# Optimization experiments

Measured on AMD Instinct MI355X. Metric: run time of the kernel, lower is better.

The kernel has to match this reference:

```python
import jax, jax.numpy as jnp
import numpy as np

H, W = 128, 128
TANX, TANY = 0.5, 0.5
SCALE_MOD = 1.0
N = 2048
T_EPS = 1e-4          # early-termination threshold used by the CUDA kernel
ALPHA_MIN = 1.0 / 255.0


def setup_inputs() -> dict:
    key = jax.random.key(0)
    ks = jax.random.split(key, 6)
    z = jax.random.uniform(ks[0], (N,), minval=2.0, maxval=6.0)
    xy = jax.random.uniform(ks[1], (N, 2), minval=-0.8, maxval=0.8) * (z[:, None] * TANX)
    means3D = jnp.concatenate([xy, z[:, None]], axis=1).astype(jnp.float32)
    means2D = jnp.zeros((N, 3), jnp.float32)  # gradient receptacle in the original API
    opacities = (jax.random.uniform(ks[2], (N, 1)) * 0.9 + 0.05).astype(jnp.float32)
    colors_precomp = jax.random.uniform(ks[3], (N, 3)).astype(jnp.float32)
    scales = jax.random.uniform(ks[4], (N, 3), minval=0.01, maxval=0.05).astype(jnp.float32)
    q = jax.random.normal(ks[5], (N, 4))
    rotations = (q / jnp.linalg.norm(q, axis=1, keepdims=True)).astype(jnp.float32)
    bg = jnp.zeros((3,), jnp.float32)
    viewmatrix = jnp.eye(4, dtype=jnp.float32)  # camera at origin looking +z (row-vector convention)
    znear, zfar = 0.01, 100.0
    P = np.zeros((4, 4), np.float32)
    P[0, 0] = 1.0 / TANX
    P[1, 1] = 1.0 / TANY
    P[2, 2] = zfar / (zfar - znear)
    P[2, 3] = -(zfar * znear) / (zfar - znear)
    P[3, 2] = 1.0
    projmatrix = jnp.asarray(P.T)  # full view@proj, row-vector convention
    return dict(bg=bg, means3D=means3D, means2D=means2D, opacities=opacities,
                colors_precomp=colors_precomp, scales=scales, rotations=rotations,
                viewmatrix=viewmatrix, projmatrix=projmatrix)


def _quat_to_rot(q):
    r, x, y, z = q[:, 0], q[:, 1], q[:, 2], q[:, 3]
    return jnp.stack([
        jnp.stack([1 - 2 * (y * y + z * z), 2 * (x * y - r * z), 2 * (x * z + r * y)], -1),
        jnp.stack([2 * (x * y + r * z), 1 - 2 * (x * x + z * z), 2 * (y * z - r * x)], -1),
        jnp.stack([2 * (x * z - r * y), 2 * (y * z + r * x), 1 - 2 * (x * x + y * y)], -1)], -2)


def _rasterize(bg, means3D, opacities, colors, scales, rotations, viewmatrix, projmatrix):
    n = means3D.shape[0]
    mh = jnp.concatenate([means3D, jnp.ones((n, 1), means3D.dtype)], 1)
    p_view = mh @ viewmatrix                 # [N,4] camera-space position
    tz = p_view[:, 2]
    p_hom = mh @ projmatrix
    p_proj = p_hom[:, :3] / (p_hom[:, 3:4] + 1e-7)
    # 3D covariance Sigma = (R S)(R S)^T
    qn = rotations / jnp.linalg.norm(rotations, axis=1, keepdims=True)
    Rm = _quat_to_rot(qn)
    M = Rm * (scales * SCALE_MOD)[:, None, :]      # R @ diag(s)
    Sigma = jnp.einsum('nij,nkj->nik', M, M)
    # EWA projection to a 2D covariance
    fx, fy = W / (2 * TANX), H / (2 * TANY)
    tx = jnp.clip(p_view[:, 0] / tz, -1.3 * TANX, 1.3 * TANX) * tz
    ty = jnp.clip(p_view[:, 1] / tz, -1.3 * TANY, 1.3 * TANY) * tz
    zero = jnp.zeros_like(tz)
    J = jnp.stack([jnp.stack([fx / tz, zero, -fx * tx / (tz * tz)], -1),
                   jnp.stack([zero, fy / tz, -fy * ty / (tz * tz)], -1)], -2)  # [N,2,3]
    Wr = viewmatrix[:3, :3]
    cov_cam = jnp.einsum('ji,njk,kl->nil', Wr, Sigma, Wr)      # W^T Sigma W
    cov2d = jnp.einsum('nij,njk,nlk->nil', J, cov_cam, J)      # [N,2,2]
    a = cov2d[:, 0, 0] + 0.3
    c = cov2d[:, 1, 1] + 0.3
    b = cov2d[:, 0, 1]
    det = a * c - b * b
    valid = (tz > 0.2) & (det > 0.0)                            # near-plane + degenerate culling
    det_s = jnp.where(det > 0.0, det, 1.0)
    conA, conB, conC = c / det_s, -b / det_s, a / det_s         # conic (inverse 2D cov)
    mid = 0.5 * (a + c)
    lam = mid + jnp.sqrt(jnp.maximum(0.1, mid * mid - det))
    radii = jnp.where(valid, jnp.ceil(3.0 * jnp.sqrt(lam)), 0.0).astype(jnp.int32)
    # NDC -> pixel coords
    px = ((p_proj[:, 0] + 1.0) * W - 1.0) * 0.5
    py = ((p_proj[:, 1] + 1.0) * H - 1.0) * 0.5
    # global front-to-back depth sort (per-tile in the CUDA kernel)
    order = jnp.argsort(tz)
    px_s, py_s = px[order], py[order]
    cA, cB, cC = conA[order], conB[order], conC[order]
    op_s = opacities[order, 0]
    col_s = colors[order]
    tz_s = tz[order]
    val_s = valid[order]
    yy, xx = jnp.meshgrid(jnp.arange(H, dtype=means3D.dtype),
                          jnp.arange(W, dtype=means3D.dtype), indexing='ij')
    gx, gy = xx.reshape(-1, 1), yy.reshape(-1, 1)   # [P,1]
    dx = px_s[None, :] - gx                          # [P,N]
    dy = py_s[None, :] - gy
    power = -0.5 * (cA[None, :] * dx * dx + cC[None, :] * dy * dy) - cB[None, :] * dx * dy
    alpha = jnp.minimum(0.99, op_s[None, :] * jnp.exp(power))
    alpha = jnp.where((power <= 0.0) & (alpha >= ALPHA_MIN) & val_s[None, :], alpha, 0.0)
    Tinc = jnp.cumprod(1.0 - alpha, axis=1)
    T = jnp.concatenate([jnp.ones((H * W, 1), alpha.dtype), Tinc[:, :-1]], axis=1)  # exclusive transmittance
    wgt = jnp.where(T > T_EPS, alpha * T, 0.0)       # early termination
    color = wgt @ col_s + Tinc[:, -1:] * bg[None, :]  # [P,3]
    depth = wgt @ tz_s                                # [P]
    counter = jnp.sum(wgt > 0.0, axis=1).astype(jnp.int32)
    color = color.reshape(H, W, 3).transpose(2, 0, 1)
    depth = depth.reshape(1, H, W)
    counter = counter.reshape(H, W)
    return color, depth, radii, counter


def reference(bg, means3D, means2D, opacities, colors_precomp, scales, rotations, viewmatrix, projmatrix):
    # means2D is only a gradient receptacle in the original API; it does not affect the math.
    return _rasterize(bg, means3D, opacities, colors_precomp, scales, rotations, viewmatrix, projmatrix)
```

## Files before the change

kernel.cpp:

```cpp
#include <hip/hip_runtime.h>
#include <math.h>

#define N_G   2048
#define W_IMG 128
#define H_IMG 128
#define NPIX  (W_IMG * H_IMG)
#define TANX  0.5f
#define TANY  0.5f
#define ALPHA_MIN (1.0f / 255.0f)
#define T_EPS_C 1e-4f
#define NTHR  1024
#define NWAVE 16

__global__ __launch_bounds__(NTHR) void gs_fused(const float* __restrict__ means3D,
                                                 const float* __restrict__ opac,
                                                 const float* __restrict__ colors,
                                                 const float* __restrict__ scales,
                                                 const float* __restrict__ rots,
                                                 const float* __restrict__ viewm,
                                                 const float* __restrict__ projm,
                                                 const float* __restrict__ bg,
                                                 float* __restrict__ out) {
    __shared__ float4 bbx[N_G];
    __shared__ float4 pf1[N_G];
    __shared__ float4 pf2[N_G];
    __shared__ unsigned short lst[N_G];
    __shared__ unsigned short srt[N_G];
    __shared__ float4 scratch4[512];
    __shared__ float4 accv[NTHR];
    __shared__ int s_count;

    float* scr = (float*)scratch4;

    int tid = threadIdx.x;
    int bid = blockIdx.x;
    float* radii_out = out + 4 * NPIX;
    if (tid == 0) s_count = 0;

#pragma unroll
    for (int k = 0; k < N_G / NTHR; k++) {
        int i = k * NTHR + tid;

        float mx = means3D[i * 3 + 0], my = means3D[i * 3 + 1], mz = means3D[i * 3 + 2];
        float pv0 = mx * viewm[0] + my * viewm[4] + mz * viewm[8]  + viewm[12];
        float pv1 = mx * viewm[1] + my * viewm[5] + mz * viewm[9]  + viewm[13];
        float tz  = mx * viewm[2] + my * viewm[6] + mz * viewm[10] + viewm[14];

        float ph[4];
#pragma unroll
        for (int j = 0; j < 4; j++)
            ph[j] = mx * projm[0 * 4 + j] + my * projm[1 * 4 + j] + mz * projm[2 * 4 + j] + projm[3 * 4 + j];
        float inv_w = __builtin_amdgcn_rcpf(ph[3] + 1e-7f);
        float ppx = ph[0] * inv_w, ppy = ph[1] * inv_w;

        float qr = rots[i * 4 + 0], qx = rots[i * 4 + 1], qy = rots[i * 4 + 2], qz = rots[i * 4 + 3];
        float qn = __builtin_amdgcn_rsqf(qr * qr + qx * qx + qy * qy + qz * qz);
        qr *= qn; qx *= qn; qy *= qn; qz *= qn;
        float R[3][3] = {
            {1.0f - 2.0f * (qy * qy + qz * qz), 2.0f * (qx * qy - qr * qz), 2.0f * (qx * qz + qr * qy)},
            {2.0f * (qx * qy + qr * qz), 1.0f - 2.0f * (qx * qx + qz * qz), 2.0f * (qy * qz - qr * qx)},
            {2.0f * (qx * qz - qr * qy), 2.0f * (qy * qz + qr * qx), 1.0f - 2.0f * (qx * qx + qy * qy)}};

        float sc[3] = {scales[i * 3 + 0], scales[i * 3 + 1], scales[i * 3 + 2]};
        float M[3][3];
#pragma unroll
        for (int r = 0; r < 3; r++)
#pragma unroll
            for (int cx = 0; cx < 3; cx++) M[r][cx] = R[r][cx] * sc[cx];

        float Sg[3][3];
#pragma unroll
        for (int r = 0; r < 3; r++)
#pragma unroll
            for (int kk = 0; kk < 3; kk++)
                Sg[r][kk] = M[r][0] * M[kk][0] + M[r][1] * M[kk][1] + M[r][2] * M[kk][2];

        float T1[3][3];
#pragma unroll
        for (int j = 0; j < 3; j++)
#pragma unroll
            for (int l = 0; l < 3; l++)
                T1[j][l] = Sg[j][0] * viewm[0 * 4 + l] + Sg[j][1] * viewm[1 * 4 + l] + Sg[j][2] * viewm[2 * 4 + l];
        float Cc[3][3];
#pragma unroll
        for (int r = 0; r < 3; r++)
#pragma unroll
            for (int l = 0; l < 3; l++)
                Cc[r][l] = viewm[0 * 4 + r] * T1[0][l] + viewm[1 * 4 + r] * T1[1][l] + viewm[2 * 4 + r] * T1[2][l];

        const float fx = W_IMG / (2.0f * TANX), fy = H_IMG / (2.0f * TANY);
        float invtz = __builtin_amdgcn_rcpf(tz);
        float txl = fminf(fmaxf(pv0 * invtz, -1.3f * TANX), 1.3f * TANX) * tz;
        float tyl = fminf(fmaxf(pv1 * invtz, -1.3f * TANY), 1.3f * TANY) * tz;
        float a0 = fx * invtz, a2 = -fx * txl * invtz * invtz;
        float b1 = fy * invtz, b2 = -fy * tyl * invtz * invtz;

        float c00 = a0 * a0 * Cc[0][0] + 2.0f * a0 * a2 * Cc[0][2] + a2 * a2 * Cc[2][2];
        float c11 = b1 * b1 * Cc[1][1] + 2.0f * b1 * b2 * Cc[1][2] + b2 * b2 * Cc[2][2];
        float c01 = a0 * b1 * Cc[0][1] + a0 * b2 * Cc[0][2] + a2 * b1 * Cc[1][2] + a2 * b2 * Cc[2][2];

        float a = c00 + 0.3f, c = c11 + 0.3f, b = c01;
        float det = a * c - b * b;
        bool valid = (tz > 0.2f) && (det > 0.0f);
        float det_s = (det > 0.0f) ? det : 1.0f;
        float rdet = __builtin_amdgcn_rcpf(det_s);
        float conA = c * rdet, conB = -b * rdet, conC = a * rdet;
        float mid = 0.5f * (a + c);
        float lam = mid + __builtin_amdgcn_sqrtf(fmaxf(0.1f, mid * mid - det));
        float radf = valid ? ceilf(3.0f * __builtin_amdgcn_sqrtf(lam)) : 0.0f;

        float op = opac[i];
        float L = __logf(255.0f * op);
        float ex, ey;
        if (valid && L > 0.0f) {
            ex = __builtin_amdgcn_sqrtf(2.0f * L * a) + 2e-2f;
            ey = __builtin_amdgcn_sqrtf(2.0f * L * c) + 2e-2f;
        } else {
            ex = -1e9f; ey = -1e9f;
        }

        bbx[i] = make_float4(((ppx + 1.0f) * (float)W_IMG - 1.0f) * 0.5f,
                             ((ppy + 1.0f) * (float)H_IMG - 1.0f) * 0.5f, ex, ey);
        pf1[i] = make_float4(conA, conB, conC, op);
        pf2[i] = make_float4(colors[i * 3 + 0], colors[i * 3 + 1], colors[i * 3 + 2], tz);

        if (bid == 0) radii_out[i] = (float)(int)radf;
    }
    __syncthreads();

    int tilex = bid & 15, tiley = bid >> 4;
    int wave = tid >> 6, lane = tid & 63;

    {
        float tx0 = (float)(tilex << 3), ty0 = (float)(tiley << 3);
        float tx1 = tx0 + 7.0f, ty1 = ty0 + 7.0f;
#pragma unroll
        for (int cc = 0; cc < 2; cc++) {
            int gi = (wave * 2 + cc) * 64 + lane;
            float4 b = bbx[gi];
            bool pred = (b.x >= tx0 - b.z) && (b.x <= tx1 + b.z) &&
                        (b.y >= ty0 - b.w) && (b.y <= ty1 + b.w);
            unsigned long long m = __ballot(pred);
            int n = (int)__popcll(m);
            int base = 0;
            if (lane == 0 && n) base = atomicAdd(&s_count, n);
            base = __shfl(base, 0);
            if (pred)
                lst[base + (int)__popcll(m & ((1ull << lane) - 1ull))] = (unsigned short)gi;
        }
    }
    __syncthreads();
    int c = s_count;

    for (int t = tid; t < c; t += NTHR) scr[t] = pf2[lst[t]].w;
    __syncthreads();
    for (int t = tid; t < c; t += NTHR) {
        int gi = lst[t];
        float my = scr[t];
        int rank = 0;
        int j = 0;
        for (; j + 4 <= c; j += 4) {
            float4 v = scratch4[j >> 2];
            int i0 = lst[j], i1 = lst[j + 1], i2 = lst[j + 2], i3 = lst[j + 3];
            rank += (v.x < my) || (v.x == my && i0 < gi);
            rank += (v.y < my) || (v.y == my && i1 < gi);
            rank += (v.z < my) || (v.z == my && i2 < gi);
            rank += (v.w < my) || (v.w == my && i3 < gi);
        }
        for (; j < c; j++) {
            float v = scr[j];
            rank += (v < my) || (v == my && lst[j] < gi);
        }
        srt[rank] = (unsigned short)gi;
    }
    __syncthreads();

    float gx = (float)((tilex << 3) + (lane & 7));
    float gy = (float)((tiley << 3) + (lane >> 3));
    int seglen = (c + NWAVE - 1) / NWAVE;
    int s0 = wave * seglen;
    int s1 = min(c, s0 + seglen);

    float Tw = 1.0f;
    for (int t = s0; t < s1; ++t) {
        int g = srt[t];
        float4 f1 = pf1[g];
        float4 b = bbx[g];
        float dx = b.x - gx, dy = b.y - gy;
        float power = -0.5f * (f1.x * dx * dx + f1.z * dy * dy) - f1.y * dx * dy;
        if (power <= 0.0f) {
            float alpha = fminf(0.99f, f1.w * __expf(power));
            if (alpha >= ALPHA_MIN) Tw *= (1.0f - alpha);
        }
    }
    scr[wave * 64 + lane] = Tw;
    __syncthreads();

    float T0 = 1.0f;
#pragma unroll
    for (int s = 0; s < NWAVE - 1; ++s) if (s < wave) T0 *= scr[s * 64 + lane];
    float T = T0, cr = 0.0f, cg = 0.0f, cb = 0.0f, dep = 0.0f;
    int cnt = 0;
    if (!__all(T0 <= T_EPS_C)) {
        for (int t = s0; t < s1; ++t) {
            int g = srt[t];
            float4 f1 = pf1[g];
            float4 f2 = pf2[g];
            float4 b = bbx[g];
            float dx = b.x - gx, dy = b.y - gy;
            float power = -0.5f * (f1.x * dx * dx + f1.z * dy * dy) - f1.y * dx * dy;
            if (power <= 0.0f) {
                float alpha = fminf(0.99f, f1.w * __expf(power));
                if (alpha >= ALPHA_MIN) {
                    if (T > T_EPS_C) {
                        float w = alpha * T;
                        cr += w * f2.x; cg += w * f2.y; cb += w * f2.z;
                        dep += w * f2.w;
                        cnt++;
                    }
                    T *= (1.0f - alpha);
                    if (__all(T <= T_EPS_C)) break;
                }
            }
        }
    }
    accv[wave * 64 + lane] = make_float4(cr, cg, cb, dep);
    ((int*)lst)[wave * 64 + lane] = cnt;
    __syncthreads();

    if (tid < 64) {
        float crr = 0.0f, cgg = 0.0f, cbb = 0.0f, dpp = 0.0f, Tf = 1.0f;
        int cnt_t = 0;
        const int* an = (const int*)lst;
#pragma unroll
        for (int s = 0; s < NWAVE; ++s) {
            float4 a = accv[s * 64 + tid];
            crr += a.x; cgg += a.y; cbb += a.z; dpp += a.w;
            cnt_t += an[s * 64 + tid];
            Tf *= scr[s * 64 + tid];
        }
        crr += Tf * bg[0]; cgg += Tf * bg[1]; cbb += Tf * bg[2];

        int pid = ((tiley << 3) + (tid >> 3)) * W_IMG + (tilex << 3) + (tid & 7);
        out[0 * NPIX + pid] = crr;
        out[1 * NPIX + pid] = cgg;
        out[2 * NPIX + pid] = cbb;
        out[3 * NPIX + pid] = dpp;
        out[4 * NPIX + N_G + pid] = (float)cnt_t;
    }
}

extern "C" void kernel_launch(void* const* d_in, const int* in_sizes, int n_in,
                              void* d_out, int out_size, void* d_ws, size_t ws_size,
                              hipStream_t stream) {
    const float* bg      = (const float*)d_in[0];
    const float* means3D = (const float*)d_in[1];
    const float* opac    = (const float*)d_in[3];
    const float* colors  = (const float*)d_in[4];
    const float* scales  = (const float*)d_in[5];
    const float* rots    = (const float*)d_in[6];
    const float* viewm   = (const float*)d_in[7];
    const float* projm   = (const float*)d_in[8];

    gs_fused<<<256, NTHR, 0, stream>>>(means3D, opac, colors, scales, rots,
                                       viewm, projm, bg, (float*)d_out);
}
```

Baseline: 17.63 us.

## Use conservative bounding boxes and compute full covariance only for tile-culled gaussians

Each block no longer runs the full 3D-to-2D covariance chain for all 2048 gaussians. It uses a cheap conservative ellipse bound (max scale squared, view-matrix norm bound) for tile culling, then computes the full conic and colour only for gaussians that pass the cull, writing them in sorted order into compact shared arrays. Radii are split so each block computes 8 gaussians' radii. The looser bound admits more candidates into the sort and blend loops. The list is capped at 1024 entries, which could drop gaussians on dense tiles.

```diff
diff --git a/kernel.cpp b/kernel.cpp
--- a/kernel.cpp
+++ b/kernel.cpp
@@ -11,6 +11,79 @@
 #define T_EPS_C 1e-4f
 #define NTHR  1024
 #define NWAVE 16
+#define CAP   1024
+
+__device__ __forceinline__ void full_chain(int i,
+        const float* __restrict__ means3D, const float* __restrict__ opac,
+        const float* __restrict__ colors, const float* __restrict__ scales,
+        const float* __restrict__ rots, const float* __restrict__ viewm,
+        const float* __restrict__ projm,
+        float4& f1, float4& f2, float& radf) {
+    float mx = means3D[i * 3 + 0], my = means3D[i * 3 + 1], mz = means3D[i * 3 + 2];
+    float pv0 = mx * viewm[0] + my * viewm[4] + mz * viewm[8]  + viewm[12];
+    float pv1 = mx * viewm[1] + my * viewm[5] + mz * viewm[9]  + viewm[13];
+    float tz  = mx * viewm[2] + my * viewm[6] + mz * viewm[10] + viewm[14];
+
+    float qr = rots[i * 4 + 0], qx = rots[i * 4 + 1], qy = rots[i * 4 + 2], qz = rots[i * 4 + 3];
+    float qn = __builtin_amdgcn_rsqf(qr * qr + qx * qx + qy * qy + qz * qz);
+    qr *= qn; qx *= qn; qy *= qn; qz *= qn;
+    float R[3][3] = {
+        {1.0f - 2.0f * (qy * qy + qz * qz), 2.0f * (qx * qy - qr * qz), 2.0f * (qx * qz + qr * qy)},
+        {2.0f * (qx * qy + qr * qz), 1.0f - 2.0f * (qx * qx + qz * qz), 2.0f * (qy * qz - qr * qx)},
+        {2.0f * (qx * qz - qr * qy), 2.0f * (qy * qz + qr * qx), 1.0f - 2.0f * (qx * qx + qy * qy)}};
+
+    float sc[3] = {scales[i * 3 + 0], scales[i * 3 + 1], scales[i * 3 + 2]};
+    float M[3][3];
+#pragma unroll
+    for (int r = 0; r < 3; r++)
+#pragma unroll
+        for (int cx = 0; cx < 3; cx++) M[r][cx] = R[r][cx] * sc[cx];
+
+    float Sg[3][3];
+#pragma unroll
+    for (int r = 0; r < 3; r++)
+#pragma unroll
+        for (int kk = 0; kk < 3; kk++)
+            Sg[r][kk] = M[r][0] * M[kk][0] + M[r][1] * M[kk][1] + M[r][2] * M[kk][2];
+
+    float T1[3][3];
+#pragma unroll
+    for (int j = 0; j < 3; j++)
+#pragma unroll
+        for (int l = 0; l < 3; l++)
+            T1[j][l] = Sg[j][0] * viewm[0 * 4 + l] + Sg[j][1] * viewm[1 * 4 + l] + Sg[j][2] * viewm[2 * 4 + l];
+    float Cc[3][3];
+#pragma unroll
+    for (int r = 0; r < 3; r++)
+#pragma unroll
+        for (int l = 0; l < 3; l++)
+            Cc[r][l] = viewm[0 * 4 + r] * T1[0][l] + viewm[1 * 4 + r] * T1[1][l] + viewm[2 * 4 + r] * T1[2][l];
+
+    const float fx = W_IMG / (2.0f * TANX), fy = H_IMG / (2.0f * TANY);
+    float invtz = __builtin_amdgcn_rcpf(tz);
+    float txl = fminf(fmaxf(pv0 * invtz, -1.3f * TANX), 1.3f * TANX) * tz;
+    float tyl = fminf(fmaxf(pv1 * invtz, -1.3f * TANY), 1.3f * TANY) * tz;
+    float a0 = fx * invtz, a2 = -fx * txl * invtz * invtz;
+    float b1 = fy * invtz, b2 = -fy * tyl * invtz * invtz;
+
+    float c00 = a0 * a0 * Cc[0][0] + 2.0f * a0 * a2 * Cc[0][2] + a2 * a2 * Cc[2][2];
+    float c11 = b1 * b1 * Cc[1][1] + 2.0f * b1 * b2 * Cc[1][2] + b2 * b2 * Cc[2][2];
+    float c01 = a0 * b1 * Cc[0][1] + a0 * b2 * Cc[0][2] + a2 * b1 * Cc[1][2] + a2 * b2 * Cc[2][2];
+
+    float a = c00 + 0.3f, c = c11 + 0.3f, b = c01;
+    float det = a * c - b * b;
+    bool valid = (tz > 0.2f) && (det > 0.0f);
+    float det_s = (det > 0.0f) ? det : 1.0f;
+    float rdet = __builtin_amdgcn_rcpf(det_s);
+    float conA = c * rdet, conB = -b * rdet, conC = a * rdet;
+    float mid = 0.5f * (a + c);
+    float lam = mid + __builtin_amdgcn_sqrtf(fmaxf(0.1f, mid * mid - det));
+    radf = valid ? ceilf(3.0f * __builtin_amdgcn_sqrtf(lam)) : 0.0f;
+
+    float op = opac[i];
+    f1 = make_float4(conA, conB, conC, valid ? op : 0.0f);
+    f2 = make_float4(colors[i * 3 + 0], colors[i * 3 + 1], colors[i * 3 + 2], tz);
+}
 
 __global__ __launch_bounds__(NTHR) void gs_fused(const float* __restrict__ means3D,
                                                  const float* __restrict__ opac,
@@ -22,25 +95,32 @@
                                                  const float* __restrict__ bg,
                                                  float* __restrict__ out) {
     __shared__ float4 bbx[N_G];
-    __shared__ float4 pf1[N_G];
-    __shared__ float4 pf2[N_G];
+    __shared__ float  tzv[N_G];
     __shared__ unsigned short lst[N_G];
-    __shared__ unsigned short srt[N_G];
-    __shared__ float4 scratch4[512];
+    __shared__ float4 sf1[CAP];
+    __shared__ float4 sf2[CAP];
+    __shared__ float2 spos[CAP];
+    __shared__ float4 scratch4[CAP / 4];
     __shared__ float4 accv[NTHR];
     __shared__ int s_count;
 
     float* scr = (float*)scratch4;
-
     int tid = threadIdx.x;
     int bid = blockIdx.x;
     float* radii_out = out + 4 * NPIX;
     if (tid == 0) s_count = 0;
 
+    float cs0 = fabsf(viewm[0]) + fabsf(viewm[4]) + fabsf(viewm[8]);
+    float cs1 = fabsf(viewm[1]) + fabsf(viewm[5]) + fabsf(viewm[9]);
+    float cs2 = fabsf(viewm[2]) + fabsf(viewm[6]) + fabsf(viewm[10]);
+    float rs0 = fabsf(viewm[0]) + fabsf(viewm[1]) + fabsf(viewm[2]);
+    float rs1 = fabsf(viewm[4]) + fabsf(viewm[5]) + fabsf(viewm[6]);
+    float rs2 = fabsf(viewm[8]) + fabsf(viewm[9]) + fabsf(viewm[10]);
+    float wb2 = fmaxf(cs0, fmaxf(cs1, cs2)) * fmaxf(rs0, fmaxf(rs1, rs2));
+
 #pragma unroll
     for (int k = 0; k < N_G / NTHR; k++) {
         int i = k * NTHR + tid;
-
         float mx = means3D[i * 3 + 0], my = means3D[i * 3 + 1], mz = means3D[i * 3 + 2];
         float pv0 = mx * viewm[0] + my * viewm[4] + mz * viewm[8]  + viewm[12];
         float pv1 = mx * viewm[1] + my * viewm[5] + mz * viewm[9]  + viewm[13];
@@ -51,80 +131,29 @@
         for (int j = 0; j < 4; j++)
             ph[j] = mx * projm[0 * 4 + j] + my * projm[1 * 4 + j] + mz * projm[2 * 4 + j] + projm[3 * 4 + j];
         float inv_w = __builtin_amdgcn_rcpf(ph[3] + 1e-7f);
-        float ppx = ph[0] * inv_w, ppy = ph[1] * inv_w;
-
-        float qr = rots[i * 4 + 0], qx = rots[i * 4 + 1], qy = rots[i * 4 + 2], qz = rots[i * 4 + 3];
-        float qn = __builtin_amdgcn_rsqf(qr * qr + qx * qx + qy * qy + qz * qz);
-        qr *= qn; qx *= qn; qy *= qn; qz *= qn;
-        float R[3][3] = {
-            {1.0f - 2.0f * (qy * qy + qz * qz), 2.0f * (qx * qy - qr * qz), 2.0f * (qx * qz + qr * qy)},
-            {2.0f * (qx * qy + qr * qz), 1.0f - 2.0f * (qx * qx + qz * qz), 2.0f * (qy * qz - qr * qx)},
-            {2.0f * (qx * qz - qr * qy), 2.0f * (qy * qz + qr * qx), 1.0f - 2.0f * (qx * qx + qy * qy)}};
-
-        float sc[3] = {scales[i * 3 + 0], scales[i * 3 + 1], scales[i * 3 + 2]};
-        float M[3][3];
-#pragma unroll
-        for (int r = 0; r < 3; r++)
-#pragma unroll
-            for (int cx = 0; cx < 3; cx++) M[r][cx] = R[r][cx] * sc[cx];
-
-        float Sg[3][3];
-#pragma unroll
-        for (int r = 0; r < 3; r++)
-#pragma unroll
-            for (int kk = 0; kk < 3; kk++)
-                Sg[r][kk] = M[r][0] * M[kk][0] + M[r][1] * M[kk][1] + M[r][2] * M[kk][2];
-
-        float T1[3][3];
-#pragma unroll
-        for (int j = 0; j < 3; j++)
-#pragma unroll
-            for (int l = 0; l < 3; l++)
-                T1[j][l] = Sg[j][0] * viewm[0 * 4 + l] + Sg[j][1] * viewm[1 * 4 + l] + Sg[j][2] * viewm[2 * 4 + l];
-        float Cc[3][3];
-#pragma unroll
-        for (int r = 0; r < 3; r++)
-#pragma unroll
-            for (int l = 0; l < 3; l++)
-                Cc[r][l] = viewm[0 * 4 + r] * T1[0][l] + viewm[1 * 4 + r] * T1[1][l] + viewm[2 * 4 + r] * T1[2][l];
-
-        const float fx = W_IMG / (2.0f * TANX), fy = H_IMG / (2.0f * TANY);
-        float invtz = __builtin_amdgcn_rcpf(tz);
-        float txl = fminf(fmaxf(pv0 * invtz, -1.3f * TANX), 1.3f * TANX) * tz;
-        float tyl = fminf(fmaxf(pv1 * invtz, -1.3f * TANY), 1.3f * TANY) * tz;
-        float a0 = fx * invtz, a2 = -fx * txl * invtz * invtz;
-        float b1 = fy * invtz, b2 = -fy * tyl * invtz * invtz;
-
-        float c00 = a0 * a0 * Cc[0][0] + 2.0f * a0 * a2 * Cc[0][2] + a2 * a2 * Cc[2][2];
-        float c11 = b1 * b1 * Cc[1][1] + 2.0f * b1 * b2 * Cc[1][2] + b2 * b2 * Cc[2][2];
-        float c01 = a0 * b1 * Cc[0][1] + a0 * b2 * Cc[0][2] + a2 * b1 * Cc[1][2] + a2 * b2 * Cc[2][2];
-
-        float a = c00 + 0.3f, c = c11 + 0.3f, b = c01;
-        float det = a * c - b * b;
-        bool valid = (tz > 0.2f) && (det > 0.0f);
-        float det_s = (det > 0.0f) ? det : 1.0f;
-        float rdet = __builtin_amdgcn_rcpf(det_s);
-        float conA = c * rdet, conB = -b * rdet, conC = a * rdet;
-        float mid = 0.5f * (a + c);
-        float lam = mid + __builtin_amdgcn_sqrtf(fmaxf(0.1f, mid * mid - det));
-        float radf = valid ? ceilf(3.0f * __builtin_amdgcn_sqrtf(lam)) : 0.0f;
-
+        float px = ((ph[0] * inv_w + 1.0f) * (float)W_IMG - 1.0f) * 0.5f;
+        float py = ((ph[1] * inv_w + 1.0f) * (float)H_IMG - 1.0f) * 0.5f;
+
+        float s0 = scales[i * 3 + 0], s1 = scales[i * 3 + 1], s2 = scales[i * 3 + 2];
+        float smax2 = fmaxf(s0 * s0, fmaxf(s1 * s1, s2 * s2));
         float op = opac[i];
         float L = __logf(255.0f * op);
-        float ex, ey;
-        if (valid && L > 0.0f) {
-            ex = __builtin_amdgcn_sqrtf(2.0f * L * a) + 2e-2f;
-            ey = __builtin_amdgcn_sqrtf(2.0f * L * c) + 2e-2f;
-        } else {
-            ex = -1e9f; ey = -1e9f;
-        }
-
-        bbx[i] = make_float4(((ppx + 1.0f) * (float)W_IMG - 1.0f) * 0.5f,
-                             ((ppy + 1.0f) * (float)H_IMG - 1.0f) * 0.5f, ex, ey);
-        pf1[i] = make_float4(conA, conB, conC, op);
-        pf2[i] = make_float4(colors[i * 3 + 0], colors[i * 3 + 1], colors[i * 3 + 2], tz);
-
-        if (bid == 0) radii_out[i] = (float)(int)radf;
+
+        float invtz = __builtin_amdgcn_rcpf(tz);
+        float ux = pv0 * invtz, uy = pv1 * invtz;
+        float u2x = fminf(ux * ux, 0.4225f);
+        float u2y = fminf(uy * uy, 0.4225f);
+        float f2 = (W_IMG / (2.0f * TANX)) * invtz;
+        f2 *= f2;
+        float sw = smax2 * wb2;
+        float abound = f2 * (1.0f + u2x) * sw + 0.3f;
+        float cbound = f2 * (1.0f + u2y) * sw + 0.3f;
+        float exb = __builtin_amdgcn_sqrtf(2.0f * L * abound) * 1.03f + 0.05f;
+        float eyb = __builtin_amdgcn_sqrtf(2.0f * L * cbound) * 1.03f + 0.05f;
+        if (!(tz > 0.2f) || !(L > 0.0f)) { exb = -1e9f; eyb = -1e9f; }
+
+        bbx[i] = make_float4(px, py, exb, eyb);
+        tzv[i] = tz;
     }
     __syncthreads();
 
@@ -150,10 +179,11 @@
         }
     }
     __syncthreads();
-    int c = s_count;
-
-    for (int t = tid; t < c; t += NTHR) scr[t] = pf2[lst[t]].w;
-    __syncthreads();
+    int c = min(s_count, CAP);
+
+    for (int t = tid; t < c; t += NTHR) scr[t] = tzv[lst[t]];
+    __syncthreads();
+
     for (int t = tid; t < c; t += NTHR) {
         int gi = lst[t];
         float my = scr[t];
@@ -171,7 +201,18 @@
             float v = scr[j];
             rank += (v < my) || (v == my && lst[j] < gi);
         }
-        srt[rank] = (unsigned short)gi;
+        float4 f1, f2v; float radf;
+        full_chain(gi, means3D, opac, colors, scales, rots, viewm, projm, f1, f2v, radf);
+        sf1[rank] = f1;
+        sf2[rank] = f2v;
+        float4 b = bbx[gi];
+        spos[rank] = make_float2(b.x, b.y);
+    }
+    if (tid < 8) {
+        int g8 = bid * 8 + tid;
+        float4 d1, d2; float radf;
+        full_chain(g8, means3D, opac, colors, scales, rots, viewm, projm, d1, d2, radf);
+        radii_out[g8] = (float)(int)radf;
     }
     __syncthreads();
 
@@ -183,10 +224,9 @@
 
     float Tw = 1.0f;
     for (int t = s0; t < s1; ++t) {
-        int g = srt[t];
-        float4 f1 = pf1[g];
-        float4 b = bbx[g];
-        float dx = b.x - gx, dy = b.y - gy;
+        float4 f1 = sf1[t];
+        float2 pp = spos[t];
+        float dx = pp.x - gx, dy = pp.y - gy;
         float power = -0.5f * (f1.x * dx * dx + f1.z * dy * dy) - f1.y * dx * dy;
         if (power <= 0.0f) {
             float alpha = fminf(0.99f, f1.w * __expf(power));
@@ -203,19 +243,18 @@
     int cnt = 0;
     if (!__all(T0 <= T_EPS_C)) {
         for (int t = s0; t < s1; ++t) {
-            int g = srt[t];
-            float4 f1 = pf1[g];
-            float4 f2 = pf2[g];
-            float4 b = bbx[g];
-            float dx = b.x - gx, dy = b.y - gy;
+            float4 f1 = sf1[t];
+            float4 f2v = sf2[t];
+            float2 pp = spos[t];
+            float dx = pp.x - gx, dy = pp.y - gy;
             float power = -0.5f * (f1.x * dx * dx + f1.z * dy * dy) - f1.y * dx * dy;
             if (power <= 0.0f) {
                 float alpha = fminf(0.99f, f1.w * __expf(power));
                 if (alpha >= ALPHA_MIN) {
                     if (T > T_EPS_C) {
                         float w = alpha * T;
-                        cr += w * f2.x; cg += w * f2.y; cb += w * f2.z;
-                        dep += w * f2.w;
+                        cr += w * f2v.x; cg += w * f2v.y; cb += w * f2v.z;
+                        dep += w * f2v.w;
                         cnt++;
                     }
                     T *= (1.0f - alpha);
```

After: 14.79 us. 1.19x faster.

## Split per-Gaussian preprocessing into separate kernel and gather sorted params into LDS

Applied to the files above, without the earlier changes.

Per-Gaussian projection and covariance work moves out of the fused kernel, where every one of the 256 tile blocks recomputed all 2048 Gaussians, into a small precompute kernel that writes to workspace. The render kernel reads those results from global memory, culls per tile, and after ranking writes each Gaussian's parameters directly into LDS in depth order, so the blend loops no longer go through an index. This removes the redundant per-block preprocessing at the cost of a second launch and global round-trips. The per-tile list is capped at 1024 entries, which could drop Gaussians in dense tiles. Opacity is now zeroed for invalid Gaussians.

```diff
diff --git a/kernel.cpp b/kernel.cpp
--- a/kernel.cpp
+++ b/kernel.cpp
@@ -11,121 +11,124 @@
 #define T_EPS_C 1e-4f
 #define NTHR  1024
 #define NWAVE 16
-
-__global__ __launch_bounds__(NTHR) void gs_fused(const float* __restrict__ means3D,
-                                                 const float* __restrict__ opac,
-                                                 const float* __restrict__ colors,
-                                                 const float* __restrict__ scales,
-                                                 const float* __restrict__ rots,
-                                                 const float* __restrict__ viewm,
-                                                 const float* __restrict__ projm,
-                                                 const float* __restrict__ bg,
-                                                 float* __restrict__ out) {
-    __shared__ float4 bbx[N_G];
-    __shared__ float4 pf1[N_G];
-    __shared__ float4 pf2[N_G];
+#define CAP   1024
+
+__global__ __launch_bounds__(64) void gs_pre(const float* __restrict__ means3D,
+                                             const float* __restrict__ opac,
+                                             const float* __restrict__ colors,
+                                             const float* __restrict__ scales,
+                                             const float* __restrict__ rots,
+                                             const float* __restrict__ viewm,
+                                             const float* __restrict__ projm,
+                                             float4* __restrict__ bb4,
+                                             float4* __restrict__ f1g,
+                                             float4* __restrict__ f2g,
+                                             float* __restrict__ radii_out) {
+    int i = blockIdx.x * 64 + threadIdx.x;
+    if (i >= N_G) return;
+
+    float mx = means3D[i * 3 + 0], my = means3D[i * 3 + 1], mz = means3D[i * 3 + 2];
+    float pv0 = mx * viewm[0] + my * viewm[4] + mz * viewm[8]  + viewm[12];
+    float pv1 = mx * viewm[1] + my * viewm[5] + mz * viewm[9]  + viewm[13];
+    float tz  = mx * viewm[2] + my * viewm[6] + mz * viewm[10] + viewm[14];
+
+    float ph[4];
+#pragma unroll
+    for (int j = 0; j < 4; j++)
+        ph[j] = mx * projm[0 * 4 + j] + my * projm[1 * 4 + j] + mz * projm[2 * 4 + j] + projm[3 * 4 + j];
+    float inv_w = __builtin_amdgcn_rcpf(ph[3] + 1e-7f);
+    float ppx = ph[0] * inv_w, ppy = ph[1] * inv_w;
+
+    float qr = rots[i * 4 + 0], qx = rots[i * 4 + 1], qy = rots[i * 4 + 2], qz = rots[i * 4 + 3];
+    float qn = __builtin_amdgcn_rsqf(qr * qr + qx * qx + qy * qy + qz * qz);
+    qr *= qn; qx *= qn; qy *= qn; qz *= qn;
+    float R[3][3] = {
+        {1.0f - 2.0f * (qy * qy + qz * qz), 2.0f * (qx * qy - qr * qz), 2.0f * (qx * qz + qr * qy)},
+        {2.0f * (qx * qy + qr * qz), 1.0f - 2.0f * (qx * qx + qz * qz), 2.0f * (qy * qz - qr * qx)},
+        {2.0f * (qx * qz - qr * qy), 2.0f * (qy * qz + qr * qx), 1.0f - 2.0f * (qx * qx + qy * qy)}};
+
+    float sc[3] = {scales[i * 3 + 0], scales[i * 3 + 1], scales[i * 3 + 2]};
+    float M[3][3];
+#pragma unroll
+    for (int r = 0; r < 3; r++)
+#pragma unroll
+        for (int cx = 0; cx < 3; cx++) M[r][cx] = R[r][cx] * sc[cx];
+
+    float Sg[3][3];
+#pragma unroll
+    for (int r = 0; r < 3; r++)
+#pragma unroll
+        for (int kk = 0; kk < 3; kk++)
+            Sg[r][kk] = M[r][0] * M[kk][0] + M[r][1] * M[kk][1] + M[r][2] * M[kk][2];
+
+    float T1[3][3];
+#pragma unroll
+    for (int j = 0; j < 3; j++)
+#pragma unroll
+        for (int l = 0; l < 3; l++)
+            T1[j][l] = Sg[j][0] * viewm[0 * 4 + l] + Sg[j][1] * viewm[1 * 4 + l] + Sg[j][2] * viewm[2 * 4 + l];
+    float Cc[3][3];
+#pragma unroll
+    for (int r = 0; r < 3; r++)
+#pragma unroll
+        for (int l = 0; l < 3; l++)
+            Cc[r][l] = viewm[0 * 4 + r] * T1[0][l] + viewm[1 * 4 + r] * T1[1][l] + viewm[2 * 4 + r] * T1[2][l];
+
+    const float fx = W_IMG / (2.0f * TANX), fy = H_IMG / (2.0f * TANY);
+    float invtz = __builtin_amdgcn_rcpf(tz);
+    float txl = fminf(fmaxf(pv0 * invtz, -1.3f * TANX), 1.3f * TANX) * tz;
+    float tyl = fminf(fmaxf(pv1 * invtz, -1.3f * TANY), 1.3f * TANY) * tz;
+    float a0 = fx * invtz, a2 = -fx * txl * invtz * invtz;
+    float b1 = fy * invtz, b2 = -fy * tyl * invtz * invtz;
+
+    float c00 = a0 * a0 * Cc[0][0] + 2.0f * a0 * a2 * Cc[0][2] + a2 * a2 * Cc[2][2];
+    float c11 = b1 * b1 * Cc[1][1] + 2.0f * b1 * b2 * Cc[1][2] + b2 * b2 * Cc[2][2];
+    float c01 = a0 * b1 * Cc[0][1] + a0 * b2 * Cc[0][2] + a2 * b1 * Cc[1][2] + a2 * b2 * Cc[2][2];
+
+    float a = c00 + 0.3f, c = c11 + 0.3f, b = c01;
+    float det = a * c - b * b;
+    bool valid = (tz > 0.2f) && (det > 0.0f);
+    float det_s = (det > 0.0f) ? det : 1.0f;
+    float rdet = __builtin_amdgcn_rcpf(det_s);
+    float conA = c * rdet, conB = -b * rdet, conC = a * rdet;
+    float mid = 0.5f * (a + c);
+    float lam = mid + __builtin_amdgcn_sqrtf(fmaxf(0.1f, mid * mid - det));
+    float radf = valid ? ceilf(3.0f * __builtin_amdgcn_sqrtf(lam)) : 0.0f;
+
+    float op = opac[i];
+    float L = __logf(255.0f * op);
+    float ex, ey;
+    if (valid && L > 0.0f) {
+        ex = __builtin_amdgcn_sqrtf(2.0f * L * a) + 2e-2f;
+        ey = __builtin_amdgcn_sqrtf(2.0f * L * c) + 2e-2f;
+    } else {
+        ex = -1e9f; ey = -1e9f;
+    }
+
+    bb4[i] = make_float4(((ppx + 1.0f) * (float)W_IMG - 1.0f) * 0.5f,
+                         ((ppy + 1.0f) * (float)H_IMG - 1.0f) * 0.5f, ex, ey);
+    f1g[i] = make_float4(conA, conB, conC, valid ? op : 0.0f);
+    f2g[i] = make_float4(colors[i * 3 + 0], colors[i * 3 + 1], colors[i * 3 + 2], tz);
+    radii_out[i] = (float)(int)radf;
+}
+
+__global__ __launch_bounds__(NTHR) void gs_render(const float4* __restrict__ bb4,
+                                                  const float4* __restrict__ f1g,
+                                                  const float4* __restrict__ f2g,
+                                                  const float* __restrict__ bg,
+                                                  float* __restrict__ out) {
     __shared__ unsigned short lst[N_G];
-    __shared__ unsigned short srt[N_G];
-    __shared__ float4 scratch4[512];
+    __shared__ float4 scratch4[256];
+    __shared__ float4 sf1[CAP];
+    __shared__ float4 sf2[CAP];
+    __shared__ float2 spos[CAP];
     __shared__ float4 accv[NTHR];
     __shared__ int s_count;
 
     float* scr = (float*)scratch4;
-
     int tid = threadIdx.x;
     int bid = blockIdx.x;
-    float* radii_out = out + 4 * NPIX;
     if (tid == 0) s_count = 0;
-
-#pragma unroll
-    for (int k = 0; k < N_G / NTHR; k++) {
-        int i = k * NTHR + tid;
-
-        float mx = means3D[i * 3 + 0], my = means3D[i * 3 + 1], mz = means3D[i * 3 + 2];
-        float pv0 = mx * viewm[0] + my * viewm[4] + mz * viewm[8]  + viewm[12];
-        float pv1 = mx * viewm[1] + my * viewm[5] + mz * viewm[9]  + viewm[13];
-        float tz  = mx * viewm[2] + my * viewm[6] + mz * viewm[10] + viewm[14];
-
-        float ph[4];
-#pragma unroll
-        for (int j = 0; j < 4; j++)
-            ph[j] = mx * projm[0 * 4 + j] + my * projm[1 * 4 + j] + mz * projm[2 * 4 + j] + projm[3 * 4 + j];
-        float inv_w = __builtin_amdgcn_rcpf(ph[3] + 1e-7f);
-        float ppx = ph[0] * inv_w, ppy = ph[1] * inv_w;
-
-        float qr = rots[i * 4 + 0], qx = rots[i * 4 + 1], qy = rots[i * 4 + 2], qz = rots[i * 4 + 3];
-        float qn = __builtin_amdgcn_rsqf(qr * qr + qx * qx + qy * qy + qz * qz);
-        qr *= qn; qx *= qn; qy *= qn; qz *= qn;
-        float R[3][3] = {
-            {1.0f - 2.0f * (qy * qy + qz * qz), 2.0f * (qx * qy - qr * qz), 2.0f * (qx * qz + qr * qy)},
-            {2.0f * (qx * qy + qr * qz), 1.0f - 2.0f * (qx * qx + qz * qz), 2.0f * (qy * qz - qr * qx)},
-            {2.0f * (qx * qz - qr * qy), 2.0f * (qy * qz + qr * qx), 1.0f - 2.0f * (qx * qx + qy * qy)}};
-
-        float sc[3] = {scales[i * 3 + 0], scales[i * 3 + 1], scales[i * 3 + 2]};
-        float M[3][3];
-#pragma unroll
-        for (int r = 0; r < 3; r++)
-#pragma unroll
-            for (int cx = 0; cx < 3; cx++) M[r][cx] = R[r][cx] * sc[cx];
-
-        float Sg[3][3];
-#pragma unroll
-        for (int r = 0; r < 3; r++)
-#pragma unroll
-            for (int kk = 0; kk < 3; kk++)
-                Sg[r][kk] = M[r][0] * M[kk][0] + M[r][1] * M[kk][1] + M[r][2] * M[kk][2];
-
-        float T1[3][3];
-#pragma unroll
-        for (int j = 0; j < 3; j++)
-#pragma unroll
-            for (int l = 0; l < 3; l++)
-                T1[j][l] = Sg[j][0] * viewm[0 * 4 + l] + Sg[j][1] * viewm[1 * 4 + l] + Sg[j][2] * viewm[2 * 4 + l];
-        float Cc[3][3];
-#pragma unroll
-        for (int r = 0; r < 3; r++)
-#pragma unroll
-            for (int l = 0; l < 3; l++)
-                Cc[r][l] = viewm[0 * 4 + r] * T1[0][l] + viewm[1 * 4 + r] * T1[1][l] + viewm[2 * 4 + r] * T1[2][l];
-
-        const float fx = W_IMG / (2.0f * TANX), fy = H_IMG / (2.0f * TANY);
-        float invtz = __builtin_amdgcn_rcpf(tz);
-        float txl = fminf(fmaxf(pv0 * invtz, -1.3f * TANX), 1.3f * TANX) * tz;
-        float tyl = fminf(fmaxf(pv1 * invtz, -1.3f * TANY), 1.3f * TANY) * tz;
-        float a0 = fx * invtz, a2 = -fx * txl * invtz * invtz;
-        float b1 = fy * invtz, b2 = -fy * tyl * invtz * invtz;
-
-        float c00 = a0 * a0 * Cc[0][0] + 2.0f * a0 * a2 * Cc[0][2] + a2 * a2 * Cc[2][2];
-        float c11 = b1 * b1 * Cc[1][1] + 2.0f * b1 * b2 * Cc[1][2] + b2 * b2 * Cc[2][2];
-        float c01 = a0 * b1 * Cc[0][1] + a0 * b2 * Cc[0][2] + a2 * b1 * Cc[1][2] + a2 * b2 * Cc[2][2];
-
-        float a = c00 + 0.3f, c = c11 + 0.3f, b = c01;
-        float det = a * c - b * b;
-        bool valid = (tz > 0.2f) && (det > 0.0f);
-        float det_s = (det > 0.0f) ? det : 1.0f;
-        float rdet = __builtin_amdgcn_rcpf(det_s);
-        float conA = c * rdet, conB = -b * rdet, conC = a * rdet;
-        float mid = 0.5f * (a + c);
-        float lam = mid + __builtin_amdgcn_sqrtf(fmaxf(0.1f, mid * mid - det));
-        float radf = valid ? ceilf(3.0f * __builtin_amdgcn_sqrtf(lam)) : 0.0f;
-
-        float op = opac[i];
-        float L = __logf(255.0f * op);
-        float ex, ey;
-        if (valid && L > 0.0f) {
-            ex = __builtin_amdgcn_sqrtf(2.0f * L * a) + 2e-2f;
-            ey = __builtin_amdgcn_sqrtf(2.0f * L * c) + 2e-2f;
-        } else {
-            ex = -1e9f; ey = -1e9f;
-        }
-
-        bbx[i] = make_float4(((ppx + 1.0f) * (float)W_IMG - 1.0f) * 0.5f,
-                             ((ppy + 1.0f) * (float)H_IMG - 1.0f) * 0.5f, ex, ey);
-        pf1[i] = make_float4(conA, conB, conC, op);
-        pf2[i] = make_float4(colors[i * 3 + 0], colors[i * 3 + 1], colors[i * 3 + 2], tz);
-
-        if (bid == 0) radii_out[i] = (float)(int)radf;
-    }
     __syncthreads();
 
     int tilex = bid & 15, tiley = bid >> 4;
@@ -137,7 +140,7 @@
 #pragma unroll
         for (int cc = 0; cc < 2; cc++) {
             int gi = (wave * 2 + cc) * 64 + lane;
-            float4 b = bbx[gi];
+            float4 b = bb4[gi];
             bool pred = (b.x >= tx0 - b.z) && (b.x <= tx1 + b.z) &&
                         (b.y >= ty0 - b.w) && (b.y <= ty1 + b.w);
             unsigned long long m = __ballot(pred);
@@ -150,10 +153,11 @@
         }
     }
     __syncthreads();
-    int c = s_count;
-
-    for (int t = tid; t < c; t += NTHR) scr[t] = pf2[lst[t]].w;
-    __syncthreads();
+    int c = min(s_count, CAP);
+
+    for (int t = tid; t < c; t += NTHR) scr[t] = f2g[lst[t]].w;
+    __syncthreads();
+
     for (int t = tid; t < c; t += NTHR) {
         int gi = lst[t];
         float my = scr[t];
@@ -171,7 +175,10 @@
             float v = scr[j];
             rank += (v < my) || (v == my && lst[j] < gi);
         }
-        srt[rank] = (unsigned short)gi;
+        sf1[rank] = f1g[gi];
+        sf2[rank] = f2g[gi];
+        float4 b = bb4[gi];
+        spos[rank] = make_float2(b.x, b.y);
     }
     __syncthreads();
 
@@ -183,10 +190,9 @@
 
     float Tw = 1.0f;
     for (int t = s0; t < s1; ++t) {
-        int g = srt[t];
-        float4 f1 = pf1[g];
-        float4 b = bbx[g];
-        float dx = b.x - gx, dy = b.y - gy;
+        float4 f1 = sf1[t];
+        float2 pp = spos[t];
+        float dx = pp.x - gx, dy = pp.y - gy;
         float power = -0.5f * (f1.x * dx * dx + f1.z * dy * dy) - f1.y * dx * dy;
         if (power <= 0.0f) {
             float alpha = fminf(0.99f, f1.w * __expf(power));
@@ -203,19 +209,18 @@
     int cnt = 0;
     if (!__all(T0 <= T_EPS_C)) {
         for (int t = s0; t < s1; ++t) {
-            int g = srt[t];
-            float4 f1 = pf1[g];
-            float4 f2 = pf2[g];
-            float4 b = bbx[g];
-            float dx = b.x - gx, dy = b.y - gy;
+            float4 f1 = sf1[t];
+            float4 f2v = sf2[t];
+            float2 pp = spos[t];
+            float dx = pp.x - gx, dy = pp.y - gy;
             float power = -0.5f * (f1.x * dx * dx + f1.z * dy * dy) - f1.y * dx * dy;
             if (power <= 0.0f) {
                 float alpha = fminf(0.99f, f1.w * __expf(power));
                 if (alpha >= ALPHA_MIN) {
                     if (T > T_EPS_C) {
                         float w = alpha * T;
-                        cr += w * f2.x; cg += w * f2.y; cb += w * f2.z;
-                        dep += w * f2.w;
+                        cr += w * f2v.x; cg += w * f2v.y; cb += w * f2v.z;
+                        dep += w * f2v.w;
                         cnt++;
                     }
                     T *= (1.0f - alpha);
@@ -262,6 +267,13 @@
     const float* viewm   = (const float*)d_in[7];
     const float* projm   = (const float*)d_in[8];
 
-    gs_fused<<<256, NTHR, 0, stream>>>(means3D, opac, colors, scales, rots,
-                                       viewm, projm, bg, (float*)d_out);
+    float* out = (float*)d_out;
+    float4* bb4 = (float4*)d_ws;
+    float4* f1g = bb4 + N_G;
+    float4* f2g = f1g + N_G;
+    float* radii_out = out + 4 * NPIX;
+
+    gs_pre<<<N_G / 64, 64, 0, stream>>>(means3D, opac, colors, scales, rots,
+                                        viewm, projm, bb4, f1g, f2g, radii_out);
+    gs_render<<<256, NTHR, 0, stream>>>(bb4, f1g, f2g, bg, out);
 }
```

Result: no change. 17.35 us (-1.6%).
